# Performance work log

Hardware: AMD Instinct MI355X
Metric: run time of the kernel (lower is better)

The kernel has to match this reference:

```python
import jax, jax.numpy as jnp
import numpy as np

# ---- static config (mirrors GptOssDecoderLayer init) ----
H = 1024      # hidden_size
HD = 64       # head_size
NQ = 16       # num_query_heads
NKV = 4       # num_key_value_heads
G = NQ // NKV # num_key_value_groups
E = 8         # num_experts
TOPK = 2      # experts_per_token
FFN = 1024    # expert intermediate (== hidden in GPT-OSS)
B, Q = 4, 128 # batch sequences, new query tokens per sequence
P, PS = 8, 128
S = P * PS    # kv length per sequence
T = B * Q     # total query tokens
SW = 128      # sliding window (layer_idx % 2 == 0 -> active)
LIMIT = 7.0   # swiglu_limit
ALPHA = 1.702
EPS = 1e-5
NEG = -1e30
SCALE = HD ** -0.5


def rmsnorm(x, w):
    return x * w * jax.lax.rsqrt(jnp.mean(x * x, axis=-1, keepdims=True) + EPS)


def setup_inputs() -> dict:
    key = jax.random.key(0)
    ks = jax.random.split(key, 16)
    hidden = jax.random.normal(ks[0], (T, H), jnp.float32)
    kv_cache = jax.random.normal(ks[1], (B * P, 2, PS, NKV, HD), jnp.float32)
    kv_page_indices = jnp.arange(B * P, dtype=jnp.int32).reshape(B, P)
    # additive causal mask: query q sits at absolute position S - Q + q
    qpos = S - Q + jnp.arange(Q)
    kpos = jnp.arange(S)
    causal = qpos[:, None] >= kpos[None, :]
    attention_mask = jnp.broadcast_to(
        jnp.where(causal, 0.0, NEG).astype(jnp.float32), (B, Q, S))
    sinks = 0.1 * jax.random.normal(ks[2], (NQ,), jnp.float32)
    w_qkv = jax.random.normal(ks[3], (H, HD * (NQ + 2 * NKV)), jnp.float32) / np.sqrt(H)
    b_qkv = jnp.zeros((HD * (NQ + 2 * NKV),), jnp.float32)
    w_o = jax.random.normal(ks[4], (NQ * HD, H), jnp.float32) / np.sqrt(NQ * HD)
    b_o = jnp.zeros((H,), jnp.float32)
    ln1_w = jnp.ones((H,), jnp.float32)
    ln2_w = jnp.ones((H,), jnp.float32)
    w_router = jax.random.normal(ks[5], (H, E), jnp.float32) / np.sqrt(H)
    b_router = jnp.zeros((E,), jnp.float32)
    w_gate_up = jax.random.normal(ks[6], (E, H, 2 * FFN), jnp.float32) / np.sqrt(H)
    b_gate_up = jnp.zeros((E, 2 * FFN), jnp.float32)
    w_down = jax.random.normal(ks[7], (E, FFN, H), jnp.float32) / np.sqrt(FFN)
    b_down = jnp.zeros((E, H), jnp.float32)
    return dict(hidden=hidden, kv_cache=kv_cache, attention_mask=attention_mask,
                kv_page_indices=kv_page_indices, sinks=sinks, w_qkv=w_qkv,
                b_qkv=b_qkv, w_o=w_o, b_o=b_o, ln1_w=ln1_w, ln2_w=ln2_w,
                w_router=w_router, b_router=b_router, w_gate_up=w_gate_up,
                b_gate_up=b_gate_up, w_down=w_down, b_down=b_down)


def reference(hidden, kv_cache, attention_mask, kv_page_indices, sinks,
              w_qkv, b_qkv, w_o, b_o, ln1_w, ln2_w, w_router, b_router,
              w_gate_up, b_gate_up, w_down, b_down):
    # ---- attention block ----
    x = rmsnorm(hidden, ln1_w)
    qkv = x @ w_qkv + b_qkv                       # [T, HD*(NQ+2*NKV)]
    q = qkv[:, :NQ * HD].reshape(B, Q, NQ, HD)
    k_new = qkv[:, NQ * HD:(NQ + NKV) * HD].reshape(B, Q, NKV, HD)
    v_new = qkv[:, (NQ + NKV) * HD:].reshape(B, Q, NKV, HD)
    # gather paged KV cache -> [B, S, NKV, HD]; write new tokens into tail slots
    pages = kv_cache[kv_page_indices]             # [B, P, 2, PS, NKV, HD]
    K = pages[:, :, 0].reshape(B, S, NKV, HD).at[:, S - Q:].set(k_new)
    V = pages[:, :, 1].reshape(B, S, NKV, HD).at[:, S - Q:].set(v_new)
    Kr = jnp.repeat(K, G, axis=2)                 # GQA expand -> [B, S, NQ, HD]
    Vr = jnp.repeat(V, G, axis=2)
    scores = jnp.einsum('bqhd,bshd->bhqs', q * SCALE, Kr) + attention_mask[:, None]
    # sliding-window (module trims pages outside the window; equivalent mask)
    qpos = S - Q + jnp.arange(Q)
    kpos = jnp.arange(S)
    win_ok = (qpos[:, None] - kpos[None, :]) < SW
    scores = jnp.where(win_ok[None, None], scores, NEG)
    m = jnp.max(scores, axis=-1)
    m = jnp.where(jnp.isinf(m) & (m < 0), 0.0, m)
    p = jnp.exp(scores - m[..., None])            # [B, NQ, Q, S]
    # attention sink joins the softmax denominator (online-softmax correction)
    denom = jnp.sum(p, axis=-1) + jnp.exp(sinks[None, :, None] - m)
    attn = jnp.einsum('bhqs,bshd->bhqd', p, Vr) / denom[..., None]
    attn = attn.transpose(0, 2, 1, 3).reshape(T, NQ * HD)
    h = hidden + attn @ w_o + b_o
    # ---- MoE block ----
    x2 = rmsnorm(h, ln2_w)
    logits = x2 @ w_router + b_router             # [T, E]
    vals, idx = jax.lax.top_k(logits, TOPK)
    wts = jax.nn.softmax(vals, axis=-1)
    comb = jnp.sum(jax.nn.one_hot(idx, E, dtype=x2.dtype) * wts[..., None], axis=1)
    gu = jnp.einsum('th,ehf->etf', x2, w_gate_up) + b_gate_up[:, None, :]
    gate = jnp.minimum(gu[..., 0::2], LIMIT)
    up = jnp.clip(gu[..., 1::2], -LIMIT, LIMIT)
    glu = gate * jax.nn.sigmoid(gate * ALPHA)
    eo = jnp.einsum('etf,efh->eth', (up + 1.0) * glu, w_down) + b_down[:, None, :]
    moe = jnp.einsum('te,eth->th', comb, eo)
    return h + moe
```

## Files before the change

kernel.cpp:

```cpp
#include <hip/hip_runtime.h>

constexpr int H    = 1024;
constexpr int HD   = 64;
constexpr int NQ   = 16;
constexpr int NKV  = 4;
constexpr int E_   = 8;
constexpr int FFN  = 1024;
constexpr int B_   = 4;
constexpr int Q_   = 128;
constexpr int P_   = 8;
constexpr int PS   = 128;
constexpr int S_   = P_ * PS;
constexpr int T_   = B_ * Q_;
constexpr int QKV_N = HD * (NQ + 2 * NKV);
constexpr float EPS   = 1e-5f;
constexpr float ALPHA = 1.702f;
constexpr float LIMIT = 7.0f;
constexpr float SCALE = 0.125f;

constexpr int MAXROWS = 1536;

typedef __attribute__((ext_vector_type(4))) float f32x4;
typedef __attribute__((ext_vector_type(8))) short s16x8;

__device__ __forceinline__ unsigned short f2bf(float f) {
    unsigned u = __float_as_uint(f);
    u += 0x7FFFu + ((u >> 16) & 1u);
    return (unsigned short)(u >> 16);
}

__global__ __launch_bounds__(256) void rmsnorm_kernel(const float* __restrict__ in,
                                                      const float* __restrict__ w,
                                                      unsigned short* __restrict__ outb,
                                                      int* __restrict__ cnt) {
    int t   = blockIdx.x;
    int tid = threadIdx.x;
    if (t == 0 && tid < E_) cnt[tid] = 0;
    float4 v = ((const float4*)(in + (size_t)t * H))[tid];
    float ss = v.x * v.x + v.y * v.y + v.z * v.z + v.w * v.w;
#pragma unroll
    for (int off = 32; off; off >>= 1) ss += __shfl_down(ss, off);
    __shared__ float partial[4];
    __shared__ float s_inv;
    if ((tid & 63) == 0) partial[tid >> 6] = ss;
    __syncthreads();
    if (tid == 0)
        s_inv = rsqrtf((partial[0] + partial[1] + partial[2] + partial[3]) * (1.0f / H) + EPS);
    __syncthreads();
    float inv = s_inv;
    float4 wv = ((const float4*)w)[tid];
    ushort4 ob;
    ob.x = f2bf(v.x * wv.x * inv); ob.y = f2bf(v.y * wv.y * inv);
    ob.z = f2bf(v.z * wv.z * inv); ob.w = f2bf(v.w * wv.w * inv);
    ((ushort4*)(outb + (size_t)t * H))[tid] = ob;
}

__global__ __launch_bounds__(256) void gemm_dense_t(const unsigned short* __restrict__ Abf,
                                                    const float* __restrict__ W,
                                                    const float* __restrict__ bias,
                                                    const float* __restrict__ resid,
                                                    float* __restrict__ C,
                                                    float* __restrict__ Cdup, int N) {
    int nb = blockIdx.x, mb = blockIdx.y * 64;
    int tid = threadIdx.x;
    int w = tid >> 6, lane = tid & 63;
    int r16 = lane & 15, kq = lane >> 4;
    int skb = tid >> 5, sn = tid & 31;

    __shared__ unsigned short Wt[2][8][32][8];

    size_t sN = (size_t)N;
    const float* wsrc = W + (size_t)(skb * 8) * sN + nb * 32 + sn;
    const unsigned short* ap = Abf + (size_t)(mb + w * 16 + r16) * 1024 + kq * 8;

    f32x4 acc[2] = {};
    float wr[8];
#pragma unroll
    for (int j = 0; j < 8; j++) wr[j] = wsrc[(size_t)j * sN];
    {
        s16x8 p;
#pragma unroll
        for (int j = 0; j < 8; j++) p[j] = (short)f2bf(wr[j]);
        *(s16x8*)&Wt[0][skb][sn][0] = p;
    }
    __syncthreads();

#pragma unroll 2
    for (int t = 0; t < 16; t++) {
        s16x8 af[2];
#pragma unroll
        for (int ks = 0; ks < 2; ks++)
            af[ks] = *(const s16x8*)(ap + t * 64 + ks * 32);
        if (t < 15) {
            const float* ws = wsrc + (size_t)(t + 1) * 64 * sN;
#pragma unroll
            for (int j = 0; j < 8; j++) wr[j] = ws[(size_t)j * sN];
        }
#pragma unroll
        for (int ks = 0; ks < 2; ks++) {
            s16x8 b0 = *(const s16x8*)&Wt[t & 1][ks * 4 + kq][r16][0];
            s16x8 b1 = *(const s16x8*)&Wt[t & 1][ks * 4 + kq][16 + r16][0];
            acc[0] = __builtin_amdgcn_mfma_f32_16x16x32_bf16(af[ks], b0, acc[0], 0, 0, 0);
            acc[1] = __builtin_amdgcn_mfma_f32_16x16x32_bf16(af[ks], b1, acc[1], 0, 0, 0);
        }
        if (t < 15) {
            s16x8 p;
#pragma unroll
            for (int j = 0; j < 8; j++) p[j] = (short)f2bf(wr[j]);
            *(s16x8*)&Wt[(t & 1) ^ 1][skb][sn][0] = p;
        }
        __syncthreads();
    }

    int row0 = mb + w * 16 + kq * 4;
#pragma unroll
    for (int nf = 0; nf < 2; nf++) {
        int col = nb * 32 + nf * 16 + r16;
        float bcol = bias[col];
#pragma unroll
        for (int r = 0; r < 4; r++) {
            int row = row0 + r;
            float v = acc[nf][r] + bcol;
            if (resid) v += resid[(size_t)row * sN + col];
            C[(size_t)row * sN + col] = v;
            if (Cdup) Cdup[(size_t)row * sN + col] = v;
        }
    }
}

__global__ __launch_bounds__(256) void attn_group_kernel(const float* __restrict__ qkv,
                                                         const float* __restrict__ kv_cache,
                                                         const int* __restrict__ page_idx,
                                                         const float* __restrict__ sinks,
                                                         unsigned short* __restrict__ attn_bf) {
    int blk = blockIdx.x;
    int kvh = blk & 3;
    int q   = (blk >> 2) & 127;
    int b   = blk >> 9;
    int t   = b * Q_ + q;
    int tid = threadIdx.x;
    int s_lo = S_ - Q_ - 127 + q;

    __shared__ __align__(16) float Vs[128][64];
    __shared__ __align__(16) float qs4[4][64];
    __shared__ float pv[4][128];
    __shared__ float sD[4];

#pragma unroll
    for (int r = 0; r < 8; r++) {
        int l = r * 256 + tid;
        int key = l >> 4, c = l & 15;
        int s = s_lo + key;
        const float* vp;
        if (s < S_ - Q_) {
            int page = page_idx[b * P_ + (s >> 7)];
            vp = kv_cache + (size_t)page * 65536 + 32768 + (size_t)(s & 127) * (NKV * HD) + kvh * HD;
        } else {
            vp = qkv + (size_t)(b * Q_ + (s - (S_ - Q_))) * QKV_N + (NQ + NKV) * HD + kvh * HD;
        }
        ((float4*)Vs[key])[c] = *(const float4*)(vp + c * 4);
    }
    {
        int hh = tid >> 6, d2 = tid & 63;
        qs4[hh][d2] = qkv[(size_t)t * QKV_N + (kvh * 4 + hh) * HD + d2];
    }
    __syncthreads();

    {
        int key = tid & 127, hp = tid >> 7;
        int s = s_lo + key;
        const float* kp;
        if (s < S_ - Q_) {
            int page = page_idx[b * P_ + (s >> 7)];
            kp = kv_cache + (size_t)page * 65536 + (size_t)(s & 127) * (NKV * HD) + kvh * HD;
        } else {
            kp = qkv + (size_t)(b * Q_ + (s - (S_ - Q_))) * QKV_N + NQ * HD + kvh * HD;
        }
        const float4* kp4 = (const float4*)kp;
        const float4* q0p = (const float4*)qs4[hp * 2];
        const float4* q1p = (const float4*)qs4[hp * 2 + 1];
        float sc0 = 0.f, sc1 = 0.f;
#pragma unroll
        for (int d4 = 0; d4 < 16; d4++) {
            float4 kk = kp4[d4];
            float4 q0 = q0p[d4], q1 = q1p[d4];
            sc0 += q0.x * kk.x + q0.y * kk.y + q0.z * kk.z + q0.w * kk.w;
            sc1 += q1.x * kk.x + q1.y * kk.y + q1.z * kk.z + q1.w * kk.w;
        }
        pv[hp * 2][key]     = sc0 * SCALE;
        pv[hp * 2 + 1][key] = sc1 * SCALE;
    }
    __syncthreads();

    {
        int wv = tid >> 6, lane = tid & 63;
        float a0 = pv[wv][lane], a1 = pv[wv][lane + 64];
        float m = fmaxf(a0, a1);
#pragma unroll
        for (int off = 32; off; off >>= 1) m = fmaxf(m, __shfl_xor(m, off));
        float p0 = __expf(a0 - m), p1 = __expf(a1 - m);
        float l = p0 + p1;
#pragma unroll
        for (int off = 32; off; off >>= 1) l += __shfl_xor(l, off);
        pv[wv][lane] = p0;
        pv[wv][lane + 64] = p1;
        if (lane == 0) sD[wv] = l + __expf(sinks[kvh * 4 + wv] - m);
    }
    __syncthreads();

    {
        int hh = tid >> 6, d2 = tid & 63;
        float a0 = 0.f, a1 = 0.f, a2 = 0.f, a3 = 0.f;
#pragma unroll 4
        for (int i = 0; i < 128; i += 4) {
            a0 += pv[hh][i]     * Vs[i][d2];
            a1 += pv[hh][i + 1] * Vs[i + 1][d2];
            a2 += pv[hh][i + 2] * Vs[i + 2][d2];
            a3 += pv[hh][i + 3] * Vs[i + 3][d2];
        }
        float acc = ((a0 + a1) + (a2 + a3)) / sD[hh];
        attn_bf[(size_t)t * (NQ * HD) + (kvh * 4 + hh) * HD + d2] = f2bf(acc);
    }
}

__global__ __launch_bounds__(256) void rms_router_kernel(const float* __restrict__ hbuf,
                                                         const float* __restrict__ ln2w,
                                                         const float* __restrict__ w_router,
                                                         const float* __restrict__ b_router,
                                                         unsigned short* __restrict__ x2bf,
                                                         int* __restrict__ ridx,
                                                         float* __restrict__ rwt,
                                                         int* __restrict__ cnt) {
    int t = blockIdx.x;
    int tid = threadIdx.x;
    float4 v = ((const float4*)(hbuf + (size_t)t * H))[tid];
    float ss = v.x * v.x + v.y * v.y + v.z * v.z + v.w * v.w;
#pragma unroll
    for (int off = 32; off; off >>= 1) ss += __shfl_down(ss, off);
    __shared__ float partial[4];
    __shared__ float s_inv;
    if ((tid & 63) == 0) partial[tid >> 6] = ss;
    __syncthreads();
    if (tid == 0)
        s_inv = rsqrtf((partial[0] + partial[1] + partial[2] + partial[3]) * (1.0f / H) + EPS);
    __syncthreads();
    float inv = s_inv;
    float4 wv = ((const float4*)ln2w)[tid];
    float4 o;
    o.x = v.x * wv.x * inv; o.y = v.y * wv.y * inv;
    o.z = v.z * wv.z * inv; o.w = v.w * wv.w * inv;
    ushort4 ob;
    ob.x = f2bf(o.x); ob.y = f2bf(o.y); ob.z = f2bf(o.z); ob.w = f2bf(o.w);
    ((ushort4*)(x2bf + (size_t)t * H))[tid] = ob;

    const float4* wr = (const float4*)(w_router + (size_t)tid * 4 * E_);
    float p[E_];
    {
        float4 r0a = wr[0], r0b = wr[1];
        float4 r1a = wr[2], r1b = wr[3];
        float4 r2a = wr[4], r2b = wr[5];
        float4 r3a = wr[6], r3b = wr[7];
        p[0] = o.x * r0a.x + o.y * r1a.x + o.z * r2a.x + o.w * r3a.x;
        p[1] = o.x * r0a.y + o.y * r1a.y + o.z * r2a.y + o.w * r3a.y;
        p[2] = o.x * r0a.z + o.y * r1a.z + o.z * r2a.z + o.w * r3a.z;
        p[3] = o.x * r0a.w + o.y * r1a.w + o.z * r2a.w + o.w * r3a.w;
        p[4] = o.x * r0b.x + o.y * r1b.x + o.z * r2b.x + o.w * r3b.x;
        p[5] = o.x * r0b.y + o.y * r1b.y + o.z * r2b.y + o.w * r3b.y;
        p[6] = o.x * r0b.z + o.y * r1b.z + o.z * r2b.z + o.w * r3b.z;
        p[7] = o.x * r0b.w + o.y * r1b.w + o.z * r2b.w + o.w * r3b.w;
    }
    __shared__ float wsum[4][E_];
    int wv2 = tid >> 6, lane = tid & 63;
#pragma unroll
    for (int e = 0; e < E_; e++) {
        float r = p[e];
#pragma unroll
        for (int off = 32; off; off >>= 1) r += __shfl_xor(r, off);
        if (lane == 0) wsum[wv2][e] = r;
    }
    __syncthreads();
    __shared__ float logits[E_];
    if (tid < E_)
        logits[tid] = wsum[0][tid] + wsum[1][tid] + wsum[2][tid] + wsum[3][tid] + b_router[tid];
    __syncthreads();
    if (tid == 0) {
        int i0 = 0; float v0 = logits[0];
        for (int ee = 1; ee < E_; ee++)
            if (logits[ee] > v0) { v0 = logits[ee]; i0 = ee; }
        int i1 = -1; float v1 = -3.4e38f;
        for (int ee = 0; ee < E_; ee++)
            if (ee != i0 && logits[ee] > v1) { v1 = logits[ee]; i1 = ee; }
        float w0 = 1.0f / (1.0f + __expf(v1 - v0));
        ridx[t * 2] = i0; ridx[t * 2 + 1] = i1;
        rwt[t * 2] = w0;  rwt[t * 2 + 1] = 1.0f - w0;
        atomicAdd(&cnt[i0], 1);
        atomicAdd(&cnt[i1], 1);
    }
}

__global__ __launch_bounds__(256) void plumb_kernel(const int* __restrict__ cnt,
                                                    const int* __restrict__ ridx,
                                                    int* __restrict__ poff,
                                                    int* __restrict__ list) {
    __shared__ int lpos[E_], lpoff[E_];
    int tid = threadIdx.x;
    if (tid == 0) {
        int run = 0;
        for (int e = 0; e < E_; e++) { lpoff[e] = run; poff[e] = run; run += (cnt[e] + 63) & ~63; }
    }
    if (tid < E_) lpos[tid] = 0;
    __syncthreads();
    for (int i = tid; i < 2 * T_; i += 256) {
        int e = ridx[i];
        int pp = atomicAdd(&lpos[e], 1);
        list[lpoff[e] + pp] = i;
    }
}

__global__ __launch_bounds__(256) void moe_gateup_t(const unsigned short* __restrict__ x2bf,
                                                    const int* __restrict__ list,
                                                    const int* __restrict__ cnt,
                                                    const int* __restrict__ poff,
                                                    const float* __restrict__ wgu,
                                                    const float* __restrict__ bgu,
                                                    unsigned short* __restrict__ act_bf) {
    int e = blockIdx.y >> 3, tl = blockIdx.y & 7;
    int n = cnt[e];
    if (tl * 128 >= n) return;
    int base = poff[e];
    int nb = blockIdx.x;
    int tid = threadIdx.x;
    int w = tid >> 6, lane = tid & 63;
    int r16 = lane & 15, kq = lane >> 4;
    int skb = tid >> 5, sn = tid & 31;

    __shared__ unsigned short Wt[2][8][32][8];

    const float* wsrc = wgu + (size_t)e * (1024 * 2048) + (size_t)(skb * 8) * 2048 + nb * 32 + sn;

    const unsigned short* ap[2];
#pragma unroll
    for (int mf = 0; mf < 2; mf++) {
        int rr = tl * 128 + w * 32 + mf * 16 + r16;
        int t2 = (rr < n) ? list[base + rr] : list[base];
        ap[mf] = x2bf + (size_t)(t2 >> 1) * 1024 + kq * 8;
    }

    f32x4 acc[2][2] = {};
    float wr[8];
#pragma unroll
    for (int j = 0; j < 8; j++) wr[j] = wsrc[(size_t)j * 2048];
    {
        s16x8 p;
#pragma unroll
        for (int j = 0; j < 8; j++) p[j] = (short)f2bf(wr[j]);
        *(s16x8*)&Wt[0][skb][sn][0] = p;
    }
    __syncthreads();

#pragma unroll 2
    for (int t = 0; t < 16; t++) {
        s16x8 af[2][2];
#pragma unroll
        for (int mf = 0; mf < 2; mf++)
#pragma unroll
            for (int ks = 0; ks < 2; ks++)
                af[mf][ks] = *(const s16x8*)(ap[mf] + t * 64 + ks * 32);
        if (t < 15) {
            const float* ws = wsrc + (size_t)(t + 1) * 64 * 2048;
#pragma unroll
            for (int j = 0; j < 8; j++) wr[j] = ws[(size_t)j * 2048];
        }
#pragma unroll
        for (int ks = 0; ks < 2; ks++) {
            s16x8 b0 = *(const s16x8*)&Wt[t & 1][ks * 4 + kq][r16][0];
            s16x8 b1 = *(const s16x8*)&Wt[t & 1][ks * 4 + kq][16 + r16][0];
#pragma unroll
            for (int mf = 0; mf < 2; mf++) {
                acc[mf][0] = __builtin_amdgcn_mfma_f32_16x16x32_bf16(af[mf][ks], b0, acc[mf][0], 0, 0, 0);
                acc[mf][1] = __builtin_amdgcn_mfma_f32_16x16x32_bf16(af[mf][ks], b1, acc[mf][1], 0, 0, 0);
            }
        }
        if (t < 15) {
            s16x8 p;
#pragma unroll
            for (int j = 0; j < 8; j++) p[j] = (short)f2bf(wr[j]);
            *(s16x8*)&Wt[(t & 1) ^ 1][skb][sn][0] = p;
        }
        __syncthreads();
    }

    int parity = r16 & 1;
#pragma unroll
    for (int mf = 0; mf < 2; mf++)
#pragma unroll
        for (int nf = 0; nf < 2; nf++) {
            int gucol = nb * 32 + nf * 16 + r16;
            float bb = bgu[(size_t)e * 2048 + gucol];
#pragma unroll
            for (int r = 0; r < 4; r++) {
                float v = acc[mf][nf][r] + bb;
                float o = __shfl_xor(v, 1);
                if (!parity) {
                    float g = fminf(v, LIMIT);
                    float u = fminf(fmaxf(o, -LIMIT), LIMIT);
                    float glu = g / (1.0f + __expf(-ALPHA * g));
                    int rr = tl * 128 + w * 32 + mf * 16 + kq * 4 + r;
                    if (rr < n)
                        act_bf[(size_t)(base + rr) * FFN + (gucol >> 1)] = f2bf((u + 1.0f) * glu);
                }
            }
        }
}

__global__ __launch_bounds__(256) void moe_down_t(const unsigned short* __restrict__ act_bf,
                                                  const int* __restrict__ list,
                                                  const int* __restrict__ cnt,
                                                  const int* __restrict__ poff,
                                                  const float* __restrict__ rwt,
                                                  const float* __restrict__ wdn,
                                                  const float* __restrict__ b_down,
                                                  float* __restrict__ out) {
    int e = blockIdx.y >> 3, tl = blockIdx.y & 7;
    int n = cnt[e];
    if (tl * 128 >= n) return;
    int base = poff[e];
    int nb = blockIdx.x;
    int z  = blockIdx.z;
    int tid = threadIdx.x;
    int w = tid >> 6, lane = tid & 63;
    int r16 = lane & 15, kq = lane >> 4;
    int skb = tid >> 5, sn = tid & 31;

    __shared__ unsigned short Wt[2][8][32][8];

    const float* wsrc = wdn + (size_t)e * (1024 * 1024) + (size_t)(z * 512 + skb * 8) * 1024 + nb * 32 + sn;
    const unsigned short* ap[2];
#pragma unroll
    for (int mf = 0; mf < 2; mf++)
        ap[mf] = act_bf + (size_t)(base + tl * 128 + w * 32 + mf * 16 + r16) * 1024 + z * 512 + kq * 8;

    f32x4 acc[2][2] = {};
    float wr[8];
#pragma unroll
    for (int j = 0; j < 8; j++) wr[j] = wsrc[(size_t)j * 1024];
    {
        s16x8 p;
#pragma unroll
        for (int j = 0; j < 8; j++) p[j] = (short)f2bf(wr[j]);
        *(s16x8*)&Wt[0][skb][sn][0] = p;
    }
    __syncthreads();

#pragma unroll 2
    for (int t = 0; t < 8; t++) {
        s16x8 af[2][2];
#pragma unroll
        for (int mf = 0; mf < 2; mf++)
#pragma unroll
            for (int ks = 0; ks < 2; ks++)
                af[mf][ks] = *(const s16x8*)(ap[mf] + t * 64 + ks * 32);
        if (t < 7) {
            const float* ws = wsrc + (size_t)(t + 1) * 64 * 1024;
#pragma unroll
            for (int j = 0; j < 8; j++) wr[j] = ws[(size_t)j * 1024];
        }
#pragma unroll
        for (int ks = 0; ks < 2; ks++) {
            s16x8 b0 = *(const s16x8*)&Wt[t & 1][ks * 4 + kq][r16][0];
            s16x8 b1 = *(const s16x8*)&Wt[t & 1][ks * 4 + kq][16 + r16][0];
#pragma unroll
            for (int mf = 0; mf < 2; mf++) {
                acc[mf][0] = __builtin_amdgcn_mfma_f32_16x16x32_bf16(af[mf][ks], b0, acc[mf][0], 0, 0, 0);
                acc[mf][1] = __builtin_amdgcn_mfma_f32_16x16x32_bf16(af[mf][ks], b1, acc[mf][1], 0, 0, 0);
            }
        }
        if (t < 7) {
            s16x8 p;
#pragma unroll
            for (int j = 0; j < 8; j++) p[j] = (short)f2bf(wr[j]);
            *(s16x8*)&Wt[(t & 1) ^ 1][skb][sn][0] = p;
        }
        __syncthreads();
    }

#pragma unroll
    for (int mf = 0; mf < 2; mf++)
#pragma unroll
        for (int r = 0; r < 4; r++) {
            int rr = tl * 128 + w * 32 + mf * 16 + kq * 4 + r;
            if (rr < n) {
                int t2 = list[base + rr];
                float sc = rwt[t2];
                float* op = out + (size_t)(t2 >> 1) * H;
#pragma unroll
                for (int nf = 0; nf < 2; nf++) {
                    int col = nb * 32 + nf * 16 + r16;
                    float v = acc[mf][nf][r] + (z == 0 ? b_down[(size_t)e * 1024 + col] : 0.0f);
                    atomicAdd(op + col, sc * v);
                }
            }
        }
}

extern "C" void kernel_launch(void* const* d_in, const int* in_sizes, int n_in,
                              void* d_out, int out_size, void* d_ws, size_t ws_size,
                              hipStream_t stream) {
    const float* hidden          = (const float*)d_in[0];
    const float* kv_cache        = (const float*)d_in[1];
    const int*   kv_page_indices = (const int*)d_in[3];
    const float* sinks           = (const float*)d_in[4];
    const float* w_qkv           = (const float*)d_in[5];
    const float* b_qkv           = (const float*)d_in[6];
    const float* w_o             = (const float*)d_in[7];
    const float* b_o             = (const float*)d_in[8];
    const float* ln1_w           = (const float*)d_in[9];
    const float* ln2_w           = (const float*)d_in[10];
    const float* w_router        = (const float*)d_in[11];
    const float* b_router        = (const float*)d_in[12];
    const float* w_gate_up       = (const float*)d_in[13];
    const float* b_gate_up       = (const float*)d_in[14];
    const float* w_down          = (const float*)d_in[15];
    const float* b_down          = (const float*)d_in[16];
    float* out = (float*)d_out;

    char* base = (char*)d_ws;
    float* qkv   = (float*)base;                       base += (size_t)T_ * QKV_N * 4;
    float* hbuf  = (float*)base;                       base += (size_t)T_ * H * 4;
    unsigned short* x_bf    = (unsigned short*)base;   base += (size_t)T_ * H * 2;
    unsigned short* x2_bf   = (unsigned short*)base;   base += (size_t)T_ * H * 2;
    unsigned short* attn_bf = (unsigned short*)base;   base += (size_t)T_ * NQ * HD * 2;
    unsigned short* act_bf  = (unsigned short*)base;   base += (size_t)(MAXROWS + 128) * FFN * 2;
    float* rwt  = (float*)base;                        base += 2 * T_ * 4;
    int*   ridx = (int*)base;                          base += 2 * T_ * 4;
    int*   cnt  = (int*)base;                          base += E_ * 4;
    int*   poff = (int*)base;                          base += E_ * 4;
    int*   list = (int*)base;                          base += MAXROWS * 4;

    rmsnorm_kernel<<<T_, 256, 0, stream>>>(hidden, ln1_w, x_bf, cnt);
    gemm_dense_t<<<dim3(QKV_N / 32, T_ / 64), 256, 0, stream>>>(
        x_bf, w_qkv, b_qkv, nullptr, qkv, nullptr, QKV_N);
    attn_group_kernel<<<B_ * Q_ * NKV, 256, 0, stream>>>(qkv, kv_cache, kv_page_indices, sinks, attn_bf);
    gemm_dense_t<<<dim3(H / 32, T_ / 64), 256, 0, stream>>>(
        attn_bf, w_o, b_o, hidden, hbuf, out, H);
    rms_router_kernel<<<T_, 256, 0, stream>>>(hbuf, ln2_w, w_router, b_router,
                                              x2_bf, ridx, rwt, cnt);
    plumb_kernel<<<1, 256, 0, stream>>>(cnt, ridx, poff, list);
    moe_gateup_t<<<dim3(FFN * 2 / 32, E_ * 8), 256, 0, stream>>>(
        x2_bf, list, cnt, poff, w_gate_up, b_gate_up, act_bf);
    moe_down_t<<<dim3(H / 32, E_ * 8, 2), 256, 0, stream>>>(
        act_bf, list, cnt, poff, rwt, w_down, b_down, out);
}
```

Measured before the change: 335.4 us.

## Deepen prefetch pipelining in GEMMs and halve MoE row tiles to 64

All three bf16 MFMA GEMM kernels now prefetch the fp32 weight slice two K-steps ahead and the activation fragments one step ahead, using double-buffered registers and a fully unrolled K loop. This hides global-load latency behind the MFMAs. The MoE gate-up and down kernels also shrink the token tile per block from 128 to 64 rows and double the grid, so there is more parallelism with uneven expert counts. In exchange, each weight tile is reloaded and converted for twice as many blocks, and register pressure rises.

```diff
diff --git a/kernel.cpp b/kernel.cpp
--- a/kernel.cpp
+++ b/kernel.cpp
@@ -73,41 +73,51 @@
     const float* wsrc = W + (size_t)(skb * 8) * sN + nb * 32 + sn;
     const unsigned short* ap = Abf + (size_t)(mb + w * 16 + r16) * 1024 + kq * 8;
 
+    float wr[2][8];
+    s16x8 af[2][2];
     f32x4 acc[2] = {};
-    float wr[8];
-#pragma unroll
-    for (int j = 0; j < 8; j++) wr[j] = wsrc[(size_t)j * sN];
+
+#pragma unroll
+    for (int j = 0; j < 8; j++) wr[0][j] = wsrc[(size_t)j * sN];
     {
         s16x8 p;
 #pragma unroll
-        for (int j = 0; j < 8; j++) p[j] = (short)f2bf(wr[j]);
+        for (int j = 0; j < 8; j++) p[j] = (short)f2bf(wr[0][j]);
         *(s16x8*)&Wt[0][skb][sn][0] = p;
     }
-    __syncthreads();
-
-#pragma unroll 2
+#pragma unroll
+    for (int j = 0; j < 8; j++) wr[1][j] = wsrc[(size_t)(64 + j) * sN];
+#pragma unroll
+    for (int ks = 0; ks < 2; ks++) af[0][ks] = *(const s16x8*)(ap + ks * 32);
+    __syncthreads();
+
+#pragma unroll
     for (int t = 0; t < 16; t++) {
-        s16x8 af[2];
-#pragma unroll
-        for (int ks = 0; ks < 2; ks++)
-            af[ks] = *(const s16x8*)(ap + t * 64 + ks * 32);
+        s16x8 b0[2], b1[2];
+#pragma unroll
+        for (int ks = 0; ks < 2; ks++) {
+            b0[ks] = *(const s16x8*)&Wt[t & 1][ks * 4 + kq][r16][0];
+            b1[ks] = *(const s16x8*)&Wt[t & 1][ks * 4 + kq][16 + r16][0];
+        }
         if (t < 15) {
-            const float* ws = wsrc + (size_t)(t + 1) * 64 * sN;
-#pragma unroll
-            for (int j = 0; j < 8; j++) wr[j] = ws[(size_t)j * sN];
+#pragma unroll
+            for (int ks = 0; ks < 2; ks++)
+                af[(t + 1) & 1][ks] = *(const s16x8*)(ap + (t + 1) * 64 + ks * 32);
+        }
+        if (t < 14) {
+#pragma unroll
+            for (int j = 0; j < 8; j++) wr[t & 1][j] = wsrc[(size_t)((t + 2) * 64 + j) * sN];
         }
 #pragma unroll
         for (int ks = 0; ks < 2; ks++) {
-            s16x8 b0 = *(const s16x8*)&Wt[t & 1][ks * 4 + kq][r16][0];
-            s16x8 b1 = *(const s16x8*)&Wt[t & 1][ks * 4 + kq][16 + r16][0];
-            acc[0] = __builtin_amdgcn_mfma_f32_16x16x32_bf16(af[ks], b0, acc[0], 0, 0, 0);
-            acc[1] = __builtin_amdgcn_mfma_f32_16x16x32_bf16(af[ks], b1, acc[1], 0, 0, 0);
+            acc[0] = __builtin_amdgcn_mfma_f32_16x16x32_bf16(af[t & 1][ks], b0[ks], acc[0], 0, 0, 0);
+            acc[1] = __builtin_amdgcn_mfma_f32_16x16x32_bf16(af[t & 1][ks], b1[ks], acc[1], 0, 0, 0);
         }
         if (t < 15) {
             s16x8 p;
 #pragma unroll
-            for (int j = 0; j < 8; j++) p[j] = (short)f2bf(wr[j]);
-            *(s16x8*)&Wt[(t & 1) ^ 1][skb][sn][0] = p;
+            for (int j = 0; j < 8; j++) p[j] = (short)f2bf(wr[(t + 1) & 1][j]);
+            *(s16x8*)&Wt[(t + 1) & 1][skb][sn][0] = p;
         }
         __syncthreads();
     }
@@ -324,9 +334,9 @@
                                                     const float* __restrict__ wgu,
                                                     const float* __restrict__ bgu,
                                                     unsigned short* __restrict__ act_bf) {
-    int e = blockIdx.y >> 3, tl = blockIdx.y & 7;
+    int e = blockIdx.y >> 4, tl = blockIdx.y & 15;
     int n = cnt[e];
-    if (tl * 128 >= n) return;
+    if (tl * 64 >= n) return;
     int base = poff[e];
     int nb = blockIdx.x;
     int tid = threadIdx.x;
@@ -337,80 +347,78 @@
     __shared__ unsigned short Wt[2][8][32][8];
 
     const float* wsrc = wgu + (size_t)e * (1024 * 2048) + (size_t)(skb * 8) * 2048 + nb * 32 + sn;
-
-    const unsigned short* ap[2];
-#pragma unroll
-    for (int mf = 0; mf < 2; mf++) {
-        int rr = tl * 128 + w * 32 + mf * 16 + r16;
-        int t2 = (rr < n) ? list[base + rr] : list[base];
-        ap[mf] = x2bf + (size_t)(t2 >> 1) * 1024 + kq * 8;
-    }
-
-    f32x4 acc[2][2] = {};
-    float wr[8];
-#pragma unroll
-    for (int j = 0; j < 8; j++) wr[j] = wsrc[(size_t)j * 2048];
+    int rr0 = tl * 64 + w * 16 + r16;
+    int t2a = (rr0 < n) ? list[base + rr0] : list[base];
+    const unsigned short* ap = x2bf + (size_t)(t2a >> 1) * 1024 + kq * 8;
+
+    float wr[2][8];
+    s16x8 af[2][2];
+    f32x4 acc[2] = {};
+
+#pragma unroll
+    for (int j = 0; j < 8; j++) wr[0][j] = wsrc[(size_t)j * 2048];
     {
         s16x8 p;
 #pragma unroll
-        for (int j = 0; j < 8; j++) p[j] = (short)f2bf(wr[j]);
+        for (int j = 0; j < 8; j++) p[j] = (short)f2bf(wr[0][j]);
         *(s16x8*)&Wt[0][skb][sn][0] = p;
     }
-    __syncthreads();
-
-#pragma unroll 2
+#pragma unroll
+    for (int j = 0; j < 8; j++) wr[1][j] = wsrc[(size_t)(64 + j) * 2048];
+#pragma unroll
+    for (int ks = 0; ks < 2; ks++) af[0][ks] = *(const s16x8*)(ap + ks * 32);
+    __syncthreads();
+
+#pragma unroll
     for (int t = 0; t < 16; t++) {
-        s16x8 af[2][2];
-#pragma unroll
-        for (int mf = 0; mf < 2; mf++)
+        s16x8 b0[2], b1[2];
+#pragma unroll
+        for (int ks = 0; ks < 2; ks++) {
+            b0[ks] = *(const s16x8*)&Wt[t & 1][ks * 4 + kq][r16][0];
+            b1[ks] = *(const s16x8*)&Wt[t & 1][ks * 4 + kq][16 + r16][0];
+        }
+        if (t < 15) {
 #pragma unroll
             for (int ks = 0; ks < 2; ks++)
-                af[mf][ks] = *(const s16x8*)(ap[mf] + t * 64 + ks * 32);
-        if (t < 15) {
-            const float* ws = wsrc + (size_t)(t + 1) * 64 * 2048;
-#pragma unroll
-            for (int j = 0; j < 8; j++) wr[j] = ws[(size_t)j * 2048];
+                af[(t + 1) & 1][ks] = *(const s16x8*)(ap + (t + 1) * 64 + ks * 32);
+        }
+        if (t < 14) {
+#pragma unroll
+            for (int j = 0; j < 8; j++) wr[t & 1][j] = wsrc[(size_t)((t + 2) * 64 + j) * 2048];
         }
 #pragma unroll
         for (int ks = 0; ks < 2; ks++) {
-            s16x8 b0 = *(const s16x8*)&Wt[t & 1][ks * 4 + kq][r16][0];
-            s16x8 b1 = *(const s16x8*)&Wt[t & 1][ks * 4 + kq][16 + r16][0];
-#pragma unroll
-            for (int mf = 0; mf < 2; mf++) {
-                acc[mf][0] = __builtin_amdgcn_mfma_f32_16x16x32_bf16(af[mf][ks], b0, acc[mf][0], 0, 0, 0);
-                acc[mf][1] = __builtin_amdgcn_mfma_f32_16x16x32_bf16(af[mf][ks], b1, acc[mf][1], 0, 0, 0);
-            }
+            acc[0] = __builtin_amdgcn_mfma_f32_16x16x32_bf16(af[t & 1][ks], b0[ks], acc[0], 0, 0, 0);
+            acc[1] = __builtin_amdgcn_mfma_f32_16x16x32_bf16(af[t & 1][ks], b1[ks], acc[1], 0, 0, 0);
         }
         if (t < 15) {
             s16x8 p;
 #pragma unroll
-            for (int j = 0; j < 8; j++) p[j] = (short)f2bf(wr[j]);
-            *(s16x8*)&Wt[(t & 1) ^ 1][skb][sn][0] = p;
+            for (int j = 0; j < 8; j++) p[j] = (short)f2bf(wr[(t + 1) & 1][j]);
+            *(s16x8*)&Wt[(t + 1) & 1][skb][sn][0] = p;
         }
         __syncthreads();
     }
 
     int parity = r16 & 1;
 #pragma unroll
-    for (int mf = 0; mf < 2; mf++)
-#pragma unroll
-        for (int nf = 0; nf < 2; nf++) {
-            int gucol = nb * 32 + nf * 16 + r16;
-            float bb = bgu[(size_t)e * 2048 + gucol];
-#pragma unroll
-            for (int r = 0; r < 4; r++) {
-                float v = acc[mf][nf][r] + bb;
-                float o = __shfl_xor(v, 1);
-                if (!parity) {
-                    float g = fminf(v, LIMIT);
-                    float u = fminf(fmaxf(o, -LIMIT), LIMIT);
-                    float glu = g / (1.0f + __expf(-ALPHA * g));
-                    int rr = tl * 128 + w * 32 + mf * 16 + kq * 4 + r;
-                    if (rr < n)
-                        act_bf[(size_t)(base + rr) * FFN + (gucol >> 1)] = f2bf((u + 1.0f) * glu);
-                }
+    for (int nf = 0; nf < 2; nf++) {
+        int gucol = nb * 32 + nf * 16 + r16;
+        float bb = bgu[(size_t)e * 2048 + gucol];
+#pragma unroll
+        for (int r = 0; r < 4; r++) {
+            float v = acc[nf][r] + bb;
+            float o = __shfl_xor(v, 1);
+            if (!parity) {
+                float g = fminf(v, LIMIT);
+                float u = fminf(fmaxf(o, -LIMIT), LIMIT);
+                float glu = g / (1.0f + __expf(-ALPHA * g));
+                int rr = tl * 64 + w * 16 + kq * 4 + r;
+                if (rr < n)
+                    act_bf[(size_t)(base + rr) * FFN + (gucol >> 1)] = f2bf((u + 1.0f) * glu);
             }
         }
+    }
 }
 
 __global__ __launch_bounds__(256) void moe_down_t(const unsigned short* __restrict__ act_bf,
@@ -421,9 +429,9 @@
                                                   const float* __restrict__ wdn,
                                                   const float* __restrict__ b_down,
                                                   float* __restrict__ out) {
-    int e = blockIdx.y >> 3, tl = blockIdx.y & 7;
+    int e = blockIdx.y >> 4, tl = blockIdx.y & 15;
     int n = cnt[e];
-    if (tl * 128 >= n) return;
+    if (tl * 64 >= n) return;
     int base = poff[e];
     int nb = blockIdx.x;
     int z  = blockIdx.z;
@@ -435,72 +443,72 @@
     __shared__ unsigned short Wt[2][8][32][8];
 
     const float* wsrc = wdn + (size_t)e * (1024 * 1024) + (size_t)(z * 512 + skb * 8) * 1024 + nb * 32 + sn;
-    const unsigned short* ap[2];
-#pragma unroll
-    for (int mf = 0; mf < 2; mf++)
-        ap[mf] = act_bf + (size_t)(base + tl * 128 + w * 32 + mf * 16 + r16) * 1024 + z * 512 + kq * 8;
-
-    f32x4 acc[2][2] = {};
-    float wr[8];
-#pragma unroll
-    for (int j = 0; j < 8; j++) wr[j] = wsrc[(size_t)j * 1024];
+    const unsigned short* ap = act_bf + (size_t)(base + tl * 64 + w * 16 + r16) * 1024 + z * 512 + kq * 8;
+
+    float wr[2][8];
+    s16x8 af[2][2];
+    f32x4 acc[2] = {};
+
+#pragma unroll
+    for (int j = 0; j < 8; j++) wr[0][j] = wsrc[(size_t)j * 1024];
     {
         s16x8 p;
 #pragma unroll
-        for (int j = 0; j < 8; j++) p[j] = (short)f2bf(wr[j]);
+        for (int j = 0; j < 8; j++) p[j] = (short)f2bf(wr[0][j]);
         *(s16x8*)&Wt[0][skb][sn][0] = p;
     }
-    __syncthreads();
-
-#pragma unroll 2
+#pragma unroll
+    for (int j = 0; j < 8; j++) wr[1][j] = wsrc[(size_t)(64 + j) * 1024];
+#pragma unroll
+    for (int ks = 0; ks < 2; ks++) af[0][ks] = *(const s16x8*)(ap + ks * 32);
+    __syncthreads();
+
+#pragma unroll
     for (int t = 0; t < 8; t++) {
-        s16x8 af[2][2];
-#pragma unroll
-        for (int mf = 0; mf < 2; mf++)
+        s16x8 b0[2], b1[2];
+#pragma unroll
+        for (int ks = 0; ks < 2; ks++) {
+            b0[ks] = *(const s16x8*)&Wt[t & 1][ks * 4 + kq][r16][0];
+            b1[ks] = *(const s16x8*)&Wt[t & 1][ks * 4 + kq][16 + r16][0];
+        }
+        if (t < 7) {
 #pragma unroll
             for (int ks = 0; ks < 2; ks++)
-                af[mf][ks] = *(const s16x8*)(ap[mf] + t * 64 + ks * 32);
-        if (t < 7) {
-            const float* ws = wsrc + (size_t)(t + 1) * 64 * 1024;
-#pragma unroll
-            for (int j = 0; j < 8; j++) wr[j] = ws[(size_t)j * 1024];
+                af[(t + 1) & 1][ks] = *(const s16x8*)(ap + (t + 1) * 64 + ks * 32);
+        }
+        if (t < 6) {
+#pragma unroll
+            for (int j = 0; j < 8; j++) wr[t & 1][j] = wsrc[(size_t)((t + 2) * 64 + j) * 1024];
         }
 #pragma unroll
         for (int ks = 0; ks < 2; ks++) {
-            s16x8 b0 = *(const s16x8*)&Wt[t & 1][ks * 4 + kq][r16][0];
-            s16x8 b1 = *(const s16x8*)&Wt[t & 1][ks * 4 + kq][16 + r16][0];
-#pragma unroll
-            for (int mf = 0; mf < 2; mf++) {
-                acc[mf][0] = __builtin_amdgcn_mfma_f32_16x16x32_bf16(af[mf][ks], b0, acc[mf][0], 0, 0, 0);
-                acc[mf][1] = __builtin_amdgcn_mfma_f32_16x16x32_bf16(af[mf][ks], b1, acc[mf][1], 0, 0, 0);
-            }
+            acc[0] = __builtin_amdgcn_mfma_f32_16x16x32_bf16(af[t & 1][ks], b0[ks], acc[0], 0, 0, 0);
+            acc[1] = __builtin_amdgcn_mfma_f32_16x16x32_bf16(af[t & 1][ks], b1[ks], acc[1], 0, 0, 0);
         }
         if (t < 7) {
             s16x8 p;
 #pragma unroll
-            for (int j = 0; j < 8; j++) p[j] = (short)f2bf(wr[j]);
-            *(s16x8*)&Wt[(t & 1) ^ 1][skb][sn][0] = p;
+            for (int j = 0; j < 8; j++) p[j] = (short)f2bf(wr[(t + 1) & 1][j]);
+            *(s16x8*)&Wt[(t + 1) & 1][skb][sn][0] = p;
         }
         __syncthreads();
     }
 
 #pragma unroll
-    for (int mf = 0; mf < 2; mf++)
-#pragma unroll
-        for (int r = 0; r < 4; r++) {
-            int rr = tl * 128 + w * 32 + mf * 16 + kq * 4 + r;
-            if (rr < n) {
-                int t2 = list[base + rr];
-                float sc = rwt[t2];
-                float* op = out + (size_t)(t2 >> 1) * H;
-#pragma unroll
-                for (int nf = 0; nf < 2; nf++) {
-                    int col = nb * 32 + nf * 16 + r16;
-                    float v = acc[mf][nf][r] + (z == 0 ? b_down[(size_t)e * 1024 + col] : 0.0f);
-                    atomicAdd(op + col, sc * v);
-                }
+    for (int r = 0; r < 4; r++) {
+        int rr = tl * 64 + w * 16 + kq * 4 + r;
+        if (rr < n) {
+            int t2 = list[base + rr];
+            float sc = rwt[t2];
+            float* op = out + (size_t)(t2 >> 1) * H;
+#pragma unroll
+            for (int nf = 0; nf < 2; nf++) {
+                int col = nb * 32 + nf * 16 + r16;
+                float v = acc[nf][r] + (z == 0 ? b_down[(size_t)e * 1024 + col] : 0.0f);
+                atomicAdd(op + col, sc * v);
             }
         }
+    }
 }
 
 extern "C" void kernel_launch(void* const* d_in, const int* in_sizes, int n_in,
@@ -546,8 +554,8 @@
     rms_router_kernel<<<T_, 256, 0, stream>>>(hbuf, ln2_w, w_router, b_router,
                                               x2_bf, ridx, rwt, cnt);
     plumb_kernel<<<1, 256, 0, stream>>>(cnt, ridx, poff, list);
-    moe_gateup_t<<<dim3(FFN * 2 / 32, E_ * 8), 256, 0, stream>>>(
+    moe_gateup_t<<<dim3(FFN * 2 / 32, E_ * 16), 256, 0, stream>>>(
         x2_bf, list, cnt, poff, w_gate_up, b_gate_up, act_bf);
-    moe_down_t<<<dim3(H / 32, E_ * 8, 2), 256, 0, stream>>>(
+    moe_down_t<<<dim3(H / 32, E_ * 16, 2), 256, 0, stream>>>(
         act_bf, list, cnt, poff, rwt, w_down, b_down, out);
 }
```

New measurement: 290.3 us. 13.4% less time.
